# Kernel tuning notes

Hardware: AMD Instinct MI355X
Metric: run time of the kernel (lower is better)

## Reference

```python
import jax, jax.numpy as jnp
import numpy as np

ALPHA = 0.2  # LeakyReLU negative slope
NEG_INF = jnp.float32(-9e15)


def gat_layer(h, mask, W, a, concat):
    """Dense GAT layer (pyGAT style). h: [B,N,Fin], mask: [N,N] bool, W: [Fin,Fout], a: [2*Fout,1]."""
    Wh = h @ W                                   # [B,N,Fout]
    F_out = W.shape[-1]
    e_src = Wh @ a[:F_out]                       # [B,N,1]
    e_dst = Wh @ a[F_out:]                       # [B,N,1]
    e = jax.nn.leaky_relu(e_src + jnp.swapaxes(e_dst, -1, -2), ALPHA)  # [B,N,N]
    att = jnp.where(mask, e, NEG_INF)
    att = jax.nn.softmax(att, axis=-1)
    out = att @ Wh                               # [B,N,Fout]
    return jax.nn.elu(out) if concat else out


def setup_inputs() -> dict:
    key = jax.random.key(0)
    ks = jax.random.split(key, 8)
    B, N, nfeat, nhid, nheads, emb, nclass = 4, 2048, 128, 64, 8, 64, 16
    slices = jax.random.normal(ks[0], (B, N, nfeat), jnp.float32)
    adj = jax.random.randint(ks[1], (N, N), 0, 2, jnp.int32)
    s = 1.0 / float(np.sqrt(nfeat))
    Ws = jax.random.uniform(ks[2], (nheads, nfeat, nhid), jnp.float32, -s, s)
    As = jax.random.uniform(ks[3], (nheads, 2 * nhid, 1), jnp.float32, -s, s)
    W1 = jax.random.uniform(ks[4], (nhid * nheads, emb), jnp.float32, -s, s)
    a1 = jax.random.uniform(ks[5], (2 * emb, 1), jnp.float32, -s, s)
    W2 = jax.random.uniform(ks[6], (emb, nclass), jnp.float32, -s, s)
    a2 = jax.random.uniform(ks[7], (2 * nclass, 1), jnp.float32, -s, s)
    return {"slices": slices, "adj": adj, "Ws": Ws, "As": As,
            "W1": W1, "a1": a1, "W2": W2, "a2": a2}


def reference(slices, adj, Ws, As, W1, a1, W2, a2):
    # Eval mode: dropout = 0 (identity).
    mask = adj > 0                               # [N,N], broadcasts over batch
    # Multi-head GAT with concat=True (ELU inside each head), vectorized over heads.
    heads = jax.vmap(lambda W, a: gat_layer(slices, mask, W, a, True))(Ws, As)  # [H,B,N,nhid]
    H, B, N, nh = heads.shape
    x = jnp.moveaxis(heads, 0, 2).reshape(B, N, H * nh)  # concat along features, head-major
    image_feature = jax.nn.elu(gat_layer(x, mask, W1, a1, False))              # [B,N,emb]
    pre = jax.nn.elu(gat_layer(image_feature, mask, W2, a2, False))            # [B,N,nclass]
    pre = pre[:, 0, :]                                                         # [B,nclass]
    return image_feature, pre
```

## Files before the change

### kernel.cpp

```cpp
#include <hip/hip_runtime.h>
#include <hip/hip_bf16.h>
#include <cstdint>


#define NN 2048

typedef float f32x4 __attribute__((ext_vector_type(4)));
typedef __bf16 bf16x8 __attribute__((ext_vector_type(8)));
typedef _Float16 f16;
typedef _Float16 f16x8 __attribute__((ext_vector_type(8)));

__global__ __launch_bounds__(256) void prep_k(
    const int* __restrict__ adj, unsigned char* __restrict__ pm,
    const float* __restrict__ Ws, __bf16* __restrict__ WsFh, __bf16* __restrict__ WsFl,
    const float* __restrict__ W1, __bf16* __restrict__ W1Fh, __bf16* __restrict__ W1Fl,
    unsigned int* __restrict__ ticket) {
  const int bx = blockIdx.x, t = threadIdx.x;
  if (bx == 0 && t == 0) *ticket = 0u;
  if (bx < 2048) {
    const int i = bx;
#pragma unroll
    for (int jt = 0; jt < 8; ++jt) {
      const int j = jt * 256 + t;
      pm[((long)(j >> 5) << 16) + i * 32 + (j & 31)] =
          adj[(long)i * NN + j] > 0 ? 0xFFu : 0u;
    }
  } else if (bx < 2304) {
    const int idx = (bx - 2048) * 256 + t;
    const int inst = idx >> 13;
    const int rem = idx & 8191;
    const int k = rem >> 6, n = rem & 63;
    const float v = Ws[(long)inst * 8192 + rem];
    const __bf16 vh = (__bf16)v;
    const int pos = ((k >> 5) * 4 + (n >> 4)) * 512 + (((k >> 3) & 3) * 16 + (n & 15)) * 8 + (k & 7);
    WsFh[(long)inst * 8192 + pos] = vh;
    WsFl[(long)inst * 8192 + pos] = (__bf16)(v - (float)vh);
  } else {
    const int idx = (bx - 2304) * 256 + t;
    const int k = idx >> 6, n = idx & 63;
    const float v = W1[idx];
    const __bf16 vh = (__bf16)v;
    const int pos = ((k >> 5) * 4 + (n >> 4)) * 512 + (((k >> 3) & 3) * 16 + (n & 15)) * 8 + (k & 7);
    W1Fh[pos] = vh;
    W1Fl[pos] = (__bf16)(v - (float)vh);
  }
}

struct GemmLd {
  float4 a0, a1;
  bf16x8 bh[4], bl[4];
};

__global__ __launch_bounds__(128) void gemm_mfma_k(
    const float* __restrict__ Aall, const __bf16* __restrict__ WFhi,
    const __bf16* __restrict__ WFlo, const float* __restrict__ avecAll,
    f16* __restrict__ WhBAll, float* __restrict__ Eo, float* __restrict__ Go,
    f16* __restrict__ Fo, f16* __restrict__ Ho,
    int K, long aStrideB) {
  const int bid = blockIdx.x;
  const int xcd = bid & 7, r = bid >> 3;
  const int xblk = r & 63, hh = r >> 6;
  const int head = ((xcd >> 2) << 2) + hh;
  const int p = (head << 2) | (xcd & 3);
  const float* A = Aall + (long)(p & 3) * aStrideB;
  const long wfOff = (long)(p >> 2) * K * 64;
  const bf16x8* BhF = (const bf16x8*)(WFhi + wfOff);
  const bf16x8* BlF = (const bf16x8*)(WFlo + wfOff);

  const int t = threadIdx.x, lane = t & 63, wave = t >> 6;
  const int quad = lane >> 4, lm = lane & 15;
  const int i0w = xblk * 32 + wave * 16;
  const float* Arow = A + (long)(i0w + lm) * K;

  f32x4 acc[4];
#pragma unroll
  for (int nt = 0; nt < 4; ++nt) acc[nt] = (f32x4){0.f, 0.f, 0.f, 0.f};

  auto LOAD = [&](GemmLd& L, int k0) {
    L.a0 = *(const float4*)(Arow + k0 + quad * 8);
    L.a1 = *(const float4*)(Arow + k0 + quad * 8 + 4);
    const int bbase = (k0 >> 5) * 256 + lane;
#pragma unroll
    for (int nt = 0; nt < 4; ++nt) {
      L.bh[nt] = BhF[bbase + nt * 64];
      L.bl[nt] = BlF[bbase + nt * 64];
    }
  };
  auto STEP = [&](const GemmLd& L) {
    const float av8[8] = {L.a0.x, L.a0.y, L.a0.z, L.a0.w, L.a1.x, L.a1.y, L.a1.z, L.a1.w};
    bf16x8 ah, al;
#pragma unroll
    for (int j = 0; j < 8; ++j) {
      const __bf16 h = (__bf16)av8[j];
      ah[j] = h;
      al[j] = (__bf16)(av8[j] - (float)h);
    }
#pragma unroll
    for (int nt = 0; nt < 4; ++nt) {
      acc[nt] = __builtin_amdgcn_mfma_f32_16x16x32_bf16(ah, L.bh[nt], acc[nt], 0, 0, 0);
      acc[nt] = __builtin_amdgcn_mfma_f32_16x16x32_bf16(al, L.bh[nt], acc[nt], 0, 0, 0);
      acc[nt] = __builtin_amdgcn_mfma_f32_16x16x32_bf16(ah, L.bl[nt], acc[nt], 0, 0, 0);
    }
  };

  GemmLd La, Lb;
  LOAD(La, 0);
  for (int k0 = 0; k0 < K; k0 += 64) {
    LOAD(Lb, k0 + 32);
    STEP(La);
    LOAD(La, (k0 + 64 < K) ? k0 + 64 : 0);
    STEP(Lb);
  }

  const float* av = avecAll + (long)(p >> 2) * 128;
  f16* WhB = WhBAll + (long)p * NN * 64;
  float* E = Eo + (long)p * NN;
  float* G = Go + (long)p * NN;
  f16* F = Fo + (long)p * NN;
  f16* Hh = Ho + (long)p * NN;

  float alo[4], ahi[4];
#pragma unroll
  for (int nt = 0; nt < 4; ++nt) {
    alo[nt] = av[nt * 16 + lm];
    ahi[nt] = av[64 + nt * 16 + lm];
  }
#pragma unroll
  for (int reg = 0; reg < 4; ++reg) {
    float es = 0.f, ed = 0.f;
#pragma unroll
    for (int nt = 0; nt < 4; ++nt) {
      es += acc[nt][reg] * alo[nt];
      ed += acc[nt][reg] * ahi[nt];
    }
#pragma unroll
    for (int m = 1; m < 16; m <<= 1) {
      es += __shfl_xor(es, m);
      ed += __shfl_xor(ed, m);
    }
    if (lm == 0) {
      const int r2 = i0w + quad * 4 + reg;
      E[r2] = __expf(es);
      G[r2] = __expf(0.2f * es);
      F[r2] = (f16)__expf(ed);
      Hh[r2] = (f16)__expf(0.2f * ed);
    }
  }

  const int r0 = i0w + quad * 4;
  const long base = ((long)(r0 >> 5) * 4) * 512 + (((r0 >> 3) & 3) * 16 + lm) * 8 + (r0 & 7);
#pragma unroll
  for (int nt = 0; nt < 4; ++nt) {
    union { f16 h[4]; uint2 u; } pk;
#pragma unroll
    for (int q = 0; q < 4; ++q) pk.h[q] = (f16)acc[nt][q];
    *(uint2*)(WhB + base + nt * 512) = pk.u;
  }
}

__global__ __launch_bounds__(512) void gemm2_k(
    const float* __restrict__ Aall, const __bf16* __restrict__ WFhi,
    const __bf16* __restrict__ WFlo, const float* __restrict__ avec,
    f16* __restrict__ WhBAll, float* __restrict__ Eo, float* __restrict__ Go,
    f16* __restrict__ Fo, f16* __restrict__ Ho) {
  const int p = blockIdx.y;
  const float* A = Aall + (long)p * NN * 512;
  const bf16x8* BhF = (const bf16x8*)WFhi;
  const bf16x8* BlF = (const bf16x8*)WFlo;
  const int t = threadIdx.x, lane = t & 63, wave = t >> 6;
  const int ks = wave & 3, rh = wave >> 2;
  const int quad = lane >> 4, lm = lane & 15;
  const int i0 = blockIdx.x * 32;
  const float* Arow = A + (long)(i0 + rh * 16 + lm) * 512;
  const int kBeg = ks * 128, kEnd = kBeg + 128;

  f32x4 acc[4];
#pragma unroll
  for (int nt = 0; nt < 4; ++nt) acc[nt] = (f32x4){0.f, 0.f, 0.f, 0.f};

  auto LOAD = [&](GemmLd& L, int k0) {
    L.a0 = *(const float4*)(Arow + k0 + quad * 8);
    L.a1 = *(const float4*)(Arow + k0 + quad * 8 + 4);
    const int bbase = (k0 >> 5) * 256 + lane;
#pragma unroll
    for (int nt = 0; nt < 4; ++nt) {
      L.bh[nt] = BhF[bbase + nt * 64];
      L.bl[nt] = BlF[bbase + nt * 64];
    }
  };
  auto STEP = [&](const GemmLd& L) {
    const float av8[8] = {L.a0.x, L.a0.y, L.a0.z, L.a0.w, L.a1.x, L.a1.y, L.a1.z, L.a1.w};
    bf16x8 ah, al;
#pragma unroll
    for (int j = 0; j < 8; ++j) {
      const __bf16 h = (__bf16)av8[j];
      ah[j] = h;
      al[j] = (__bf16)(av8[j] - (float)h);
    }
#pragma unroll
    for (int nt = 0; nt < 4; ++nt) {
      acc[nt] = __builtin_amdgcn_mfma_f32_16x16x32_bf16(ah, L.bh[nt], acc[nt], 0, 0, 0);
      acc[nt] = __builtin_amdgcn_mfma_f32_16x16x32_bf16(al, L.bh[nt], acc[nt], 0, 0, 0);
      acc[nt] = __builtin_amdgcn_mfma_f32_16x16x32_bf16(ah, L.bl[nt], acc[nt], 0, 0, 0);
    }
  };

  GemmLd La, Lb;
  LOAD(La, kBeg);
  for (int k0 = kBeg; k0 < kEnd; k0 += 64) {
    LOAD(Lb, k0 + 32);
    STEP(La);
    LOAD(La, (k0 + 64 < kEnd) ? k0 + 64 : kBeg);
    STEP(Lb);
  }

  __shared__ __align__(16) float red[8][4][64][4];
#pragma unroll
  for (int nt = 0; nt < 4; ++nt) *(f32x4*)&red[wave][nt][lane][0] = acc[nt];
  __syncthreads();

  const int n = lane, rgrp = wave;
  const int rh2 = rgrp >> 2, q2 = rgrp & 3;
  const int ln = q2 * 16 + (n & 15), ntq = n >> 4;
  f32x4 c4 = *(const f32x4*)&red[rh2 * 4 + 0][ntq][ln][0];
#pragma unroll
  for (int ksum = 1; ksum < 4; ++ksum)
    c4 += *(const f32x4*)&red[rh2 * 4 + ksum][ntq][ln][0];

  f32x4 es4 = c4 * avec[n];
  f32x4 ed4 = c4 * avec[64 + n];
#pragma unroll
  for (int m = 1; m < 64; m <<= 1) {
#pragma unroll
    for (int q = 0; q < 4; ++q) {
      es4[q] += __shfl_xor(es4[q], m);
      ed4[q] += __shfl_xor(ed4[q], m);
    }
  }
  const int row0 = i0 + rgrp * 4;
  if (n == 0) {
#pragma unroll
    for (int reg = 0; reg < 4; ++reg) {
      const int row = row0 + reg;
      Eo[(long)p * NN + row] = __expf(es4[reg]);
      Go[(long)p * NN + row] = __expf(0.2f * es4[reg]);
      Fo[(long)p * NN + row] = (f16)__expf(ed4[reg]);
      Ho[(long)p * NN + row] = (f16)__expf(0.2f * ed4[reg]);
    }
  }
  f16* WhB = WhBAll + (long)p * NN * 64;
  union { f16 h[4]; uint2 u; } pk;
#pragma unroll
  for (int reg = 0; reg < 4; ++reg) pk.h[reg] = (f16)c4[reg];
  const long pos = ((long)(row0 >> 5) * 4 + ntq) * 512 +
                   ((((row0 >> 3) & 3) * 16 + (n & 15)) * 8) + (row0 & 7);
  *(uint2*)(WhB + pos) = pk.u;
}

struct KbLd {
  f16x8 F8, H8;
  f16x8 b[4];
  uint2 m[2];
};

__global__ __launch_bounds__(512, 2) void attn_k(
    const f16* __restrict__ WhBAll, const float* __restrict__ Eb,
    const float* __restrict__ Gb, const f16* __restrict__ Fb,
    const f16* __restrict__ Hb, const unsigned char* __restrict__ pm,
    float* __restrict__ out1, int rowStride, long strideB,
    int jsCount, float* __restrict__ partAcc, float* __restrict__ partSum) {
  const int bid = blockIdx.x;
  int p, js, rowblk;
  if (jsCount == 1) {
    const int xcd = bid & 7, r = bid >> 3;
    p = xcd * 4 + (r & 3);
    rowblk = r >> 2;
    js = 0;
  } else {
    const int xcd = bid & 7;
    const int idx = ((xcd & 1) << 5) + (bid >> 3);
    p = xcd >> 1;
    js = idx >> 4;
    rowblk = idx & 15;
  }
  const f16* WhB = WhBAll + (long)p * NN * 64;
  const float* E = Eb + (long)p * NN;
  const float* G = Gb + (long)p * NN;
  const f16* Fg = Fb + (long)p * NN;
  const f16* Hg = Hb + (long)p * NN;
  const int t = threadIdx.x, lane = t & 63, wave = t >> 6;
  const int rw = wave & 3, half = wave >> 2;
  const int quad = lane >> 4, lm = lane & 15;
  const int i0 = rowblk * 128;
  const int rbase = rw * 32;
  const int span = 64 / jsCount;
  const int nIter = span / 2;
  const int kbBeg = js * span + half * nIter, kbEnd = kbBeg + nIter;

  __shared__ __align__(16) float cmb[10240];

  f16x8 ev[2], gv[2];
#pragma unroll
  for (int g = 0; g < 2; ++g) {
    const int r = i0 + rbase + g * 16 + lm;
    const f16 e = (f16)E[r], gg = (f16)G[r];
#pragma unroll
    for (int j = 0; j < 8; ++j) { ev[g][j] = e; gv[g][j] = gg; }
  }

  f16x8 ones;
#pragma unroll
  for (int j = 0; j < 8; ++j) ones[j] = (lm == 0) ? (f16)1.0f : (f16)0.0f;

  f32x4 acc[2][4], sum[2];
#pragma unroll
  for (int g = 0; g < 2; ++g) {
    sum[g] = (f32x4){0.f, 0.f, 0.f, 0.f};
#pragma unroll
    for (int nt = 0; nt < 4; ++nt) acc[g][nt] = (f32x4){0.f, 0.f, 0.f, 0.f};
  }

  const unsigned char* mp[2];
#pragma unroll
  for (int g = 0; g < 2; ++g)
    mp[g] = pm + (long)(i0 + rbase + g * 16 + lm) * 32 + quad * 8;

  auto LD = [&](KbLd& L, int kb) {
    L.F8 = *(const f16x8*)(Fg + kb * 32 + quad * 8);
    L.H8 = *(const f16x8*)(Hg + kb * 32 + quad * 8);
#pragma unroll
    for (int nt = 0; nt < 4; ++nt)
      L.b[nt] = *(const f16x8*)(WhB + (long)kb * 2048 + (nt * 64 + lane) * 8);
#pragma unroll
    for (int g = 0; g < 2; ++g)
      L.m[g] = *(const uint2*)(mp[g] + ((long)kb << 16));
  };
  auto CP = [&](const KbLd& L) {
    union { f16x8 v; uint4 u4; } A[2];
#pragma unroll
    for (int g = 0; g < 2; ++g) {
      A[g].v = __builtin_elementwise_max(ev[g] * L.F8, gv[g] * L.H8);
      A[g].u4.x &= __builtin_amdgcn_perm(0u, L.m[g].x, 0x01010000u);
      A[g].u4.y &= __builtin_amdgcn_perm(0u, L.m[g].x, 0x03030202u);
      A[g].u4.z &= __builtin_amdgcn_perm(0u, L.m[g].y, 0x01010000u);
      A[g].u4.w &= __builtin_amdgcn_perm(0u, L.m[g].y, 0x03030202u);
    }
    __builtin_amdgcn_s_setprio(1);
#pragma unroll
    for (int nt = 0; nt < 4; ++nt) {
#pragma unroll
      for (int g = 0; g < 2; ++g)
        acc[g][nt] = __builtin_amdgcn_mfma_f32_16x16x32_f16(A[g].v, L.b[nt], acc[g][nt], 0, 0, 0);
    }
#pragma unroll
    for (int g = 0; g < 2; ++g)
      sum[g] = __builtin_amdgcn_mfma_f32_16x16x32_f16(A[g].v, ones, sum[g], 0, 0, 0);
    __builtin_amdgcn_s_setprio(0);
  };

  KbLd La, Lb2, Lc, Ld;
  LD(La, kbBeg);
  LD(Lb2, kbBeg + 1);
  LD(Lc, kbBeg + 2);
  LD(Ld, kbBeg + 3);
  for (int kb = kbBeg; kb < kbEnd; kb += 4) {
    CP(La);
    if (kb + 4 < kbEnd) LD(La, kb + 4);
    CP(Lb2);
    if (kb + 5 < kbEnd) LD(Lb2, kb + 5);
    CP(Lc);
    if (kb + 6 < kbEnd) LD(Lc, kb + 6);
    CP(Ld);
    if (kb + 7 < kbEnd) LD(Ld, kb + 7);
  }

  if (half == 1) {
#pragma unroll
    for (int g = 0; g < 2; ++g) {
#pragma unroll
      for (int nt = 0; nt < 4; ++nt)
        *(f32x4*)&cmb[((rw * 10 + g * 4 + nt) * 64 + lane) * 4] = acc[g][nt];
      *(f32x4*)&cmb[((rw * 10 + 8 + g) * 64 + lane) * 4] = sum[g];
    }
  }
  __syncthreads();
  if (half == 1) return;
#pragma unroll
  for (int g = 0; g < 2; ++g) {
#pragma unroll
    for (int nt = 0; nt < 4; ++nt)
      acc[g][nt] += *(const f32x4*)&cmb[((rw * 10 + g * 4 + nt) * 64 + lane) * 4];
    sum[g] += *(const f32x4*)&cmb[((rw * 10 + 8 + g) * 64 + lane) * 4];
  }

  if (jsCount == 1) {
#pragma unroll
    for (int g = 0; g < 2; ++g) {
#pragma unroll
      for (int reg = 0; reg < 4; ++reg) {
        const int row = i0 + rbase + g * 16 + quad * 4 + reg;
        const float ls = __shfl(sum[g][reg], quad * 16);
        const float il = ls > 0.f ? 1.f / ls : 0.f;
#pragma unroll
        for (int nt = 0; nt < 4; ++nt) {
          float v = acc[g][nt][reg] * il;
          v = v > 0.f ? v : expm1f(v);
          const long o = (long)(p & 3) * strideB + (long)row * rowStride + (p >> 2) * 64 + nt * 16 + lm;
          out1[o] = v;
        }
      }
    }
  } else {
    float* pAcc = partAcc + ((long)p * jsCount + js) * NN * 64;
    float* pSum = partSum + ((long)p * jsCount + js) * NN;
#pragma unroll
    for (int g = 0; g < 2; ++g) {
#pragma unroll
      for (int reg = 0; reg < 4; ++reg) {
        const int row = i0 + rbase + g * 16 + quad * 4 + reg;
#pragma unroll
        for (int nt = 0; nt < 4; ++nt) pAcc[(long)row * 64 + nt * 16 + lm] = acc[g][nt][reg];
        if (lm == 0) pSum[row] = sum[g][reg];
      }
    }
  }
}

__global__ __launch_bounds__(256) void combine_k(const float* __restrict__ partAcc,
                                                 const float* __restrict__ partSum,
                                                 float* __restrict__ img,
                                                 float* __restrict__ out, int JS) {
  const long idx = (long)blockIdx.x * 256 + threadIdx.x;
  const int cg = idx & 15;
  const int row = (int)((idx >> 4) & (NN - 1));
  const int inst = (int)(idx >> 15);
  f32x4 v = (f32x4){0.f, 0.f, 0.f, 0.f};
  float s = 0.f;
  for (int js = 0; js < JS; ++js) {
    const long b = ((long)inst * JS + js) * NN;
    v += *(const f32x4*)(partAcc + (b + row) * 64 + cg * 4);
    s += partSum[b + row];
  }
  const float il = s > 0.f ? 1.f / s : 0.f;
  f32x4 r;
#pragma unroll
  for (int q = 0; q < 4; ++q) {
    float x = v[q] * il;
    r[q] = x > 0.f ? x : expm1f(x);
  }
  const long o = ((long)inst * NN + row) * 64 + cg * 4;
  *(f32x4*)(img + o) = r;
  *(f32x4*)(out + o) = r;
}

__global__ __launch_bounds__(256) void layer3a_k(
    const float* __restrict__ img, const float* __restrict__ W2,
    const float* __restrict__ a2, const unsigned char* __restrict__ pm,
    float* __restrict__ pOut , float* __restrict__ outPre,
    unsigned int* __restrict__ ticket) {
  const int bb = blockIdx.x, chunk = blockIdx.y, t = threadIdx.x;
  const float* A = img + (long)bb * NN * 64;
  __shared__ float w2alo[64], w2ahi[64];
  __shared__ float W2s[64][17];
  __shared__ float redc[4][17];
  __shared__ int lastS;
  if (t < 64) {
    float sl = 0.f, sh = 0.f;
#pragma unroll
    for (int c = 0; c < 16; ++c) {
      const float wv = W2[t * 16 + c];
      W2s[t][c] = wv;
      sl += wv * a2[c];
      sh += wv * a2[16 + c];
    }
    w2alo[t] = sl;
    w2ahi[t] = sh;
  }
  __syncthreads();

  float es = 0.f;
#pragma unroll 16
  for (int k = 0; k < 64; ++k) es += A[k] * w2alo[k];

  const int j = chunk * 256 + t;
  float arow[64];
#pragma unroll
  for (int q = 0; q < 16; ++q) *(f32x4*)(arow + q * 4) = *(const f32x4*)(A + (long)j * 64 + q * 4);
  float ed = 0.f;
#pragma unroll
  for (int k = 0; k < 64; ++k) ed += arow[k] * w2ahi[k];
  float e = es + ed;
  e = fmaxf(e, 0.2f * e);
  const float pv = pm[((long)(j >> 5) << 16) + (j & 31)] ? __expf(e) : 0.f;

  float acc[16];
#pragma unroll
  for (int c = 0; c < 16; ++c) {
    float wh = 0.f;
#pragma unroll
    for (int k = 0; k < 64; ++k) wh += arow[k] * W2s[k][c];
    acc[c] = pv * wh;
  }
  float lsum = pv;

#pragma unroll
  for (int off = 32; off > 0; off >>= 1) {
    lsum += __shfl_down(lsum, off);
#pragma unroll
    for (int c = 0; c < 16; ++c) acc[c] += __shfl_down(acc[c], off);
  }
  if ((t & 63) == 0) {
    const int wv = t >> 6;
#pragma unroll
    for (int c = 0; c < 16; ++c) redc[wv][c] = acc[c];
    redc[wv][16] = lsum;
  }
  __syncthreads();
  if (t < 17) {
    __hip_atomic_store(&pOut[((long)bb * 8 + chunk) * 17 + t],
                       redc[0][t] + redc[1][t] + redc[2][t] + redc[3][t],
                       __ATOMIC_RELAXED, __HIP_MEMORY_SCOPE_AGENT);
  }
  __syncthreads();
  if (t == 0)
    lastS = (__hip_atomic_fetch_add(ticket, 1u, __ATOMIC_ACQ_REL,
                                    __HIP_MEMORY_SCOPE_AGENT) == 31u);
  __syncthreads();
  if (lastS && t < 64) {
    const int b2 = t >> 4, c2 = t & 15;
    float a = 0.f, l = 0.f;
#pragma unroll
    for (int ch = 0; ch < 8; ++ch) {
      a += __hip_atomic_load(&pOut[((long)b2 * 8 + ch) * 17 + c2],
                             __ATOMIC_RELAXED, __HIP_MEMORY_SCOPE_AGENT);
      l += __hip_atomic_load(&pOut[((long)b2 * 8 + ch) * 17 + 16],
                             __ATOMIC_RELAXED, __HIP_MEMORY_SCOPE_AGENT);
    }
    float v = a / l;
    v = v > 0.f ? v : expm1f(v);
    outPre[b2 * 16 + c2] = v;
  }
}

extern "C" void kernel_launch(void* const* d_in, const int* in_sizes, int n_in,
                              void* d_out, int out_size, void* d_ws, size_t ws_size,
                              hipStream_t stream) {
  (void)in_sizes; (void)n_in; (void)out_size; (void)ws_size;
  constexpr int B = 4, N = NN, JS2 = 4;

  const float* slices = (const float*)d_in[0];
  const int* adj = (const int*)d_in[1];
  const float* Ws = (const float*)d_in[2];
  const float* As = (const float*)d_in[3];
  const float* W1 = (const float*)d_in[4];
  const float* a1 = (const float*)d_in[5];
  const float* W2 = (const float*)d_in[6];
  const float* a2 = (const float*)d_in[7];
  float* out = (float*)d_out;

  char* w = (char*)d_ws;
  size_t off = 0;
  auto alloc = [&](size_t bytes) {
    void* ptr = w + off;
    off += (bytes + 255) & ~(size_t)255;
    return ptr;
  };
  unsigned char* pm = (unsigned char*)alloc((size_t)64 * 65536);
  __bf16* WsFh = (__bf16*)alloc((size_t)8 * 128 * 64 * 2);
  __bf16* WsFl = (__bf16*)alloc((size_t)8 * 128 * 64 * 2);
  __bf16* W1Fh = (__bf16*)alloc((size_t)512 * 64 * 2);
  __bf16* W1Fl = (__bf16*)alloc((size_t)512 * 64 * 2);
  f16* WhB1 = (f16*)alloc((size_t)32 * N * 64 * 2);
  float* E1 = (float*)alloc((size_t)32 * N * 4);
  float* G1 = (float*)alloc((size_t)32 * N * 4);
  f16* F1 = (f16*)alloc((size_t)32 * N * 2);
  f16* H1 = (f16*)alloc((size_t)32 * N * 2);
  float* x = (float*)alloc((size_t)B * N * 512 * 4);
  f16* WhB2 = (f16*)alloc((size_t)B * N * 64 * 2);
  float* E2 = (float*)alloc((size_t)B * N * 4);
  float* G2 = (float*)alloc((size_t)B * N * 4);
  f16* F2 = (f16*)alloc((size_t)B * N * 2);
  f16* H2 = (f16*)alloc((size_t)B * N * 2);
  float* img = (float*)alloc((size_t)B * N * 64 * 4);
  float* pAcc2 = (float*)alloc((size_t)B * JS2 * N * 64 * 4);
  float* pSum2 = (float*)alloc((size_t)B * JS2 * N * 4);
  float* pL3 = (float*)alloc((size_t)B * 8 * 17 * 4);
  unsigned int* ticket = (unsigned int*)alloc(256);

  prep_k<<<dim3(2432), dim3(256), 0, stream>>>(adj, pm, Ws, WsFh, WsFl, W1, W1Fh, W1Fl, ticket);

  gemm_mfma_k<<<dim3(2048), dim3(128), 0, stream>>>(
      slices, WsFh, WsFl, As, WhB1, E1, G1, F1, H1, 128, (long)N * 128);
  attn_k<<<dim3(512), dim3(512), 0, stream>>>(
      WhB1, E1, G1, F1, H1, pm, x, 512, (long)N * 512,
      1, (float*)nullptr, (float*)nullptr);

  gemm2_k<<<dim3(N / 32, 4), dim3(512), 0, stream>>>(
      x, W1Fh, W1Fl, a1, WhB2, E2, G2, F2, H2);
  attn_k<<<dim3(256), dim3(512), 0, stream>>>(
      WhB2, E2, G2, F2, H2, pm, (float*)nullptr, 64, (long)N * 64,
      JS2, pAcc2, pSum2);
  combine_k<<<dim3(B * N * 16 / 256), dim3(256), 0, stream>>>(pAcc2, pSum2, img, out, JS2);

  layer3a_k<<<dim3(B, 8), dim3(256), 0, stream>>>(img, W2, a2, pm, pL3,
                                                  out + (size_t)B * N * 64, ticket);
}
```

Baseline: 168.8 us.

## Pack adjacency mask into bits with LDS lookup and shallower prefetch

The adjacency mask goes from one byte per element to one bit per element, so the mask buffer is an eighth of its former size. The attention kernel now reads one byte per 8 columns and expands it into a half-precision AND mask through a 256-entry LDS lookup table. This replaces the v_perm expansion and cuts mask load traffic. The prefetch pipeline also shrinks from four in-flight key blocks to two, with sched_barrier fences, which lowers register pressure but leaves less latency hiding. The layer-3 kernel is updated to read the bit-packed mask.

```diff
diff --git a/kernel.cpp b/kernel.cpp
--- a/kernel.cpp
+++ b/kernel.cpp
@@ -11,7 +11,7 @@
 typedef _Float16 f16x8 __attribute__((ext_vector_type(8)));
 
 __global__ __launch_bounds__(256) void prep_k(
-    const int* __restrict__ adj, unsigned char* __restrict__ pm,
+    const int* __restrict__ adj, unsigned char* __restrict__ pmb,
     const float* __restrict__ Ws, __bf16* __restrict__ WsFh, __bf16* __restrict__ WsFl,
     const float* __restrict__ W1, __bf16* __restrict__ W1Fh, __bf16* __restrict__ W1Fl,
     unsigned int* __restrict__ ticket) {
@@ -19,12 +19,12 @@
   if (bx == 0 && t == 0) *ticket = 0u;
   if (bx < 2048) {
     const int i = bx;
-#pragma unroll
-    for (int jt = 0; jt < 8; ++jt) {
-      const int j = jt * 256 + t;
-      pm[((long)(j >> 5) << 16) + i * 32 + (j & 31)] =
-          adj[(long)i * NN + j] > 0 ? 0xFFu : 0u;
-    }
+    const int j0 = t * 8;
+    unsigned byte = 0;
+#pragma unroll
+    for (int b = 0; b < 8; ++b)
+      byte |= (adj[(long)i * NN + j0 + b] > 0 ? 1u : 0u) << b;
+    pmb[(j0 >> 5) * 8192 + i * 4 + ((j0 >> 3) & 3)] = (unsigned char)byte;
   } else if (bx < 2304) {
     const int idx = (bx - 2048) * 256 + t;
     const int inst = idx >> 13;
@@ -260,13 +260,13 @@
 struct KbLd {
   f16x8 F8, H8;
   f16x8 b[4];
-  uint2 m[2];
+  unsigned mb[2];
 };
 
 __global__ __launch_bounds__(512, 2) void attn_k(
     const f16* __restrict__ WhBAll, const float* __restrict__ Eb,
     const float* __restrict__ Gb, const f16* __restrict__ Fb,
-    const f16* __restrict__ Hb, const unsigned char* __restrict__ pm,
+    const f16* __restrict__ Hb, const unsigned char* __restrict__ pmb,
     float* __restrict__ out1, int rowStride, long strideB,
     int jsCount, float* __restrict__ partAcc, float* __restrict__ partSum) {
   const int bid = blockIdx.x;
@@ -298,6 +298,18 @@
   const int kbBeg = js * span + half * nIter, kbEnd = kbBeg + nIter;
 
   __shared__ __align__(16) float cmb[10240];
+  __shared__ __align__(16) uint4 lut[256];
+
+  if (t < 256) {
+    uint4 w;
+    unsigned* wp = (unsigned*)&w;
+#pragma unroll
+    for (int i2 = 0; i2 < 4; ++i2)
+      wp[i2] = (((t >> (2 * i2)) & 1) ? 0x0000FFFFu : 0u) |
+               (((t >> (2 * i2 + 1)) & 1) ? 0xFFFF0000u : 0u);
+    lut[t] = w;
+  }
+  __syncthreads();
 
   f16x8 ev[2], gv[2];
 #pragma unroll
@@ -320,10 +332,10 @@
     for (int nt = 0; nt < 4; ++nt) acc[g][nt] = (f32x4){0.f, 0.f, 0.f, 0.f};
   }
 
-  const unsigned char* mp[2];
+  const unsigned char* mpb[2];
 #pragma unroll
   for (int g = 0; g < 2; ++g)
-    mp[g] = pm + (long)(i0 + rbase + g * 16 + lm) * 32 + quad * 8;
+    mpb[g] = pmb + (long)(i0 + rbase + g * 16 + lm) * 4 + quad;
 
   auto LD = [&](KbLd& L, int kb) {
     L.F8 = *(const f16x8*)(Fg + kb * 32 + quad * 8);
@@ -333,18 +345,17 @@
       L.b[nt] = *(const f16x8*)(WhB + (long)kb * 2048 + (nt * 64 + lane) * 8);
 #pragma unroll
     for (int g = 0; g < 2; ++g)
-      L.m[g] = *(const uint2*)(mp[g] + ((long)kb << 16));
+      L.mb[g] = mpb[g][(long)kb * 8192];
   };
   auto CP = [&](const KbLd& L) {
+    const uint4 mx0 = lut[L.mb[0]];
+    const uint4 mx1 = lut[L.mb[1]];
     union { f16x8 v; uint4 u4; } A[2];
 #pragma unroll
-    for (int g = 0; g < 2; ++g) {
+    for (int g = 0; g < 2; ++g)
       A[g].v = __builtin_elementwise_max(ev[g] * L.F8, gv[g] * L.H8);
-      A[g].u4.x &= __builtin_amdgcn_perm(0u, L.m[g].x, 0x01010000u);
-      A[g].u4.y &= __builtin_amdgcn_perm(0u, L.m[g].x, 0x03030202u);
-      A[g].u4.z &= __builtin_amdgcn_perm(0u, L.m[g].y, 0x01010000u);
-      A[g].u4.w &= __builtin_amdgcn_perm(0u, L.m[g].y, 0x03030202u);
-    }
+    A[0].u4.x &= mx0.x; A[0].u4.y &= mx0.y; A[0].u4.z &= mx0.z; A[0].u4.w &= mx0.w;
+    A[1].u4.x &= mx1.x; A[1].u4.y &= mx1.y; A[1].u4.z &= mx1.z; A[1].u4.w &= mx1.w;
     __builtin_amdgcn_s_setprio(1);
 #pragma unroll
     for (int nt = 0; nt < 4; ++nt) {
@@ -358,20 +369,15 @@
     __builtin_amdgcn_s_setprio(0);
   };
 
-  KbLd La, Lb2, Lc, Ld;
+  KbLd La, Lb2;
   LD(La, kbBeg);
-  LD(Lb2, kbBeg + 1);
-  LD(Lc, kbBeg + 2);
-  LD(Ld, kbBeg + 3);
-  for (int kb = kbBeg; kb < kbEnd; kb += 4) {
+  for (int kb = kbBeg; kb < kbEnd; kb += 2) {
+    LD(Lb2, kb + 1);
+    __builtin_amdgcn_sched_barrier(0);
     CP(La);
-    if (kb + 4 < kbEnd) LD(La, kb + 4);
+    if (kb + 2 < kbEnd) LD(La, kb + 2);
+    __builtin_amdgcn_sched_barrier(0);
     CP(Lb2);
-    if (kb + 5 < kbEnd) LD(Lb2, kb + 5);
-    CP(Lc);
-    if (kb + 6 < kbEnd) LD(Lc, kb + 6);
-    CP(Ld);
-    if (kb + 7 < kbEnd) LD(Ld, kb + 7);
   }
 
   if (half == 1) {
@@ -455,7 +461,7 @@
 
 __global__ __launch_bounds__(256) void layer3a_k(
     const float* __restrict__ img, const float* __restrict__ W2,
-    const float* __restrict__ a2, const unsigned char* __restrict__ pm,
+    const float* __restrict__ a2, const unsigned char* __restrict__ pmb,
     float* __restrict__ pOut , float* __restrict__ outPre,
     unsigned int* __restrict__ ticket) {
   const int bb = blockIdx.x, chunk = blockIdx.y, t = threadIdx.x;
@@ -491,7 +497,8 @@
   for (int k = 0; k < 64; ++k) ed += arow[k] * w2ahi[k];
   float e = es + ed;
   e = fmaxf(e, 0.2f * e);
-  const float pv = pm[((long)(j >> 5) << 16) + (j & 31)] ? __expf(e) : 0.f;
+  const float pv =
+      ((pmb[(j >> 5) * 8192 + ((j >> 3) & 3)] >> (j & 7)) & 1) ? __expf(e) : 0.f;
 
   float acc[16];
 #pragma unroll
@@ -565,7 +572,7 @@
     off += (bytes + 255) & ~(size_t)255;
     return ptr;
   };
-  unsigned char* pm = (unsigned char*)alloc((size_t)64 * 65536);
+  unsigned char* pmb = (unsigned char*)alloc((size_t)64 * 8192);
   __bf16* WsFh = (__bf16*)alloc((size_t)8 * 128 * 64 * 2);
   __bf16* WsFl = (__bf16*)alloc((size_t)8 * 128 * 64 * 2);
   __bf16* W1Fh = (__bf16*)alloc((size_t)512 * 64 * 2);
@@ -587,21 +594,21 @@
   float* pL3 = (float*)alloc((size_t)B * 8 * 17 * 4);
   unsigned int* ticket = (unsigned int*)alloc(256);
 
-  prep_k<<<dim3(2432), dim3(256), 0, stream>>>(adj, pm, Ws, WsFh, WsFl, W1, W1Fh, W1Fl, ticket);
+  prep_k<<<dim3(2432), dim3(256), 0, stream>>>(adj, pmb, Ws, WsFh, WsFl, W1, W1Fh, W1Fl, ticket);
 
   gemm_mfma_k<<<dim3(2048), dim3(128), 0, stream>>>(
       slices, WsFh, WsFl, As, WhB1, E1, G1, F1, H1, 128, (long)N * 128);
   attn_k<<<dim3(512), dim3(512), 0, stream>>>(
-      WhB1, E1, G1, F1, H1, pm, x, 512, (long)N * 512,
+      WhB1, E1, G1, F1, H1, pmb, x, 512, (long)N * 512,
       1, (float*)nullptr, (float*)nullptr);
 
   gemm2_k<<<dim3(N / 32, 4), dim3(512), 0, stream>>>(
       x, W1Fh, W1Fl, a1, WhB2, E2, G2, F2, H2);
   attn_k<<<dim3(256), dim3(512), 0, stream>>>(
-      WhB2, E2, G2, F2, H2, pm, (float*)nullptr, 64, (long)N * 64,
+      WhB2, E2, G2, F2, H2, pmb, (float*)nullptr, 64, (long)N * 64,
       JS2, pAcc2, pSum2);
   combine_k<<<dim3(B * N * 16 / 256), dim3(256), 0, stream>>>(pAcc2, pSum2, img, out, JS2);
 
-  layer3a_k<<<dim3(B, 8), dim3(256), 0, stream>>>(img, W2, a2, pm, pL3,
+  layer3a_k<<<dim3(B, 8), dim3(256), 0, stream>>>(img, W2, a2, pmb, pL3,
                                                   out + (size_t)B * N * 64, ticket);
 }
```

Result: faster. 164.7 us (-2.4%).
